# Performance work log

Hardware: AMD Instinct MI355X
Metric: run time of the kernel (lower is better)

Reference implementation:

```python
import jax, jax.numpy as jnp
import numpy as np

B, D, N, MH, MV = 4, 1024, 2048, 1024, 1024

def setup_inputs() -> dict:
    key = jax.random.key(0)
    k1, k2, k3, k4, k5 = jax.random.split(key, 5)
    return {
        "x": jax.random.normal(k1, (B, D, N), dtype=jnp.float32),
        "W_Q": jax.random.normal(k2, (MH, D), dtype=jnp.float32),
        "W_K": jax.random.normal(k3, (MH, D), dtype=jnp.float32),
        "W_V": jax.random.normal(k4, (MV, D), dtype=jnp.float32),
        "W_O": jax.random.normal(k5, (D, MV), dtype=jnp.float32),
    }

def reference(x, W_Q, W_K, W_V, W_O):
    # x: [b, d, n] (feature-major). Projections: [b, m, n]
    q = jnp.einsum('hd,bdn->bhn', W_Q, x)
    k = jnp.einsum('hd,bdn->bhn', W_K, x)
    v = jnp.einsum('vd,bdn->bvn', W_V, x)
    # scores[b,i,j] = sum_h k[b,h,i] * q[b,h,j]  -> [b, n, n]; NOTE: no 1/sqrt scale (faithful)
    scores = jnp.einsum('bhi,bhj->bij', k, q)
    scores = jax.nn.softmax(scores, axis=-1)
    # v @ scores -> [b, m_V, n]
    attn = jnp.einsum('bvi,bij->bvj', v, scores)
    # W_O @ attn -> [b, d, n]
    return jnp.einsum('dv,bvj->bdj', W_O, attn)
```

## Files before the change

### kernel.cpp

```cpp
#include <hip/hip_runtime.h>
#include <cstddef>
#include <cstdint>

typedef unsigned short u16;
typedef __attribute__((ext_vector_type(8))) short bf16x8;
typedef __attribute__((ext_vector_type(8))) _Float16 f16x8;
typedef __attribute__((ext_vector_type(4))) float f32x4;
typedef __attribute__((ext_vector_type(16))) float f32x16;

#define GLOBAL_AS __attribute__((address_space(1)))
#define LDS_AS __attribute__((address_space(3)))

__device__ __forceinline__ void async16(const u16* g, u16* l) {
    __builtin_amdgcn_global_load_lds((GLOBAL_AS const uint32_t*)g,
                                     (LDS_AS uint32_t*)l, 16, 0, 0);
}

__device__ __forceinline__ u16 f2bf(float f) {
    uint32_t u = __builtin_bit_cast(uint32_t, f);
    uint32_t r = (u + 0x7FFFu + ((u >> 16) & 1u)) >> 16;
    return (u16)r;
}

__global__ __launch_bounds__(256)
void wcast(const float4* __restrict__ src, u16* __restrict__ dst)
{
    int i = blockIdx.x * 256 + threadIdx.x;
    float4 v = src[i];
    ushort4 a = { f2bf(v.x), f2bf(v.y), f2bf(v.z), f2bf(v.w) };
    *(ushort4*)&dst[4 * (size_t)i] = a;
}

__global__ __launch_bounds__(256)
void tsplit_h2(const float* __restrict__ Sb, size_t sBatch,
               u16* __restrict__ Db, size_t dBatch, size_t plane,
               int R, int C)
{
    const float* S = Sb + blockIdx.z * sBatch;
    u16* D = Db + blockIdx.z * dBatch;
    __shared__ float t[32][33];
    int tx = threadIdx.x & 31, ty = threadIdx.x >> 5;
    int c0 = blockIdx.x * 32, r0 = blockIdx.y * 32;
    #pragma unroll
    for (int k = 0; k < 4; ++k)
        t[ty + 8 * k][tx] = S[(size_t)(r0 + ty + 8 * k) * C + c0 + tx];
    __syncthreads();
    #pragma unroll
    for (int k = 0; k < 4; ++k) {
        float a = t[tx][ty + 8 * k] * 64.0f;
        _Float16 h0 = (_Float16)a;
        _Float16 h1 = (_Float16)(a - (float)h0);
        size_t o = (size_t)(c0 + ty + 8 * k) * R + r0 + tx;
        D[o] = __builtin_bit_cast(u16, h0);
        D[plane + o] = __builtin_bit_cast(u16, h1);
    }
}

__global__ __launch_bounds__(256)
void xprep(const float* __restrict__ Sb, size_t sBatch,
           u16* __restrict__ BFb, size_t bfBatch,
           u16* __restrict__ Db, size_t dBatch, size_t plane)
{
    const float* S = Sb + blockIdx.z * sBatch;
    u16* BF = BFb + blockIdx.z * bfBatch;
    u16* D = Db + blockIdx.z * dBatch;
    __shared__ float t[32][33];
    int tx = threadIdx.x & 31, ty = threadIdx.x >> 5;
    int c0 = blockIdx.x * 32, r0 = blockIdx.y * 32;
    #pragma unroll
    for (int k = 0; k < 4; ++k) {
        float v = S[(size_t)(r0 + ty + 8 * k) * 2048 + c0 + tx];
        t[ty + 8 * k][tx] = v;
        BF[(size_t)(r0 + ty + 8 * k) * 2048 + c0 + tx] = f2bf(v);
    }
    __syncthreads();
    #pragma unroll
    for (int k = 0; k < 4; ++k) {
        float a = t[tx][ty + 8 * k] * 64.0f;
        _Float16 h0 = (_Float16)a;
        _Float16 h1 = (_Float16)(a - (float)h0);
        size_t o = (size_t)(c0 + ty + 8 * k) * 1024 + r0 + tx;
        D[o] = __builtin_bit_cast(u16, h0);
        D[plane + o] = __builtin_bit_cast(u16, h1);
    }
}

__global__ __launch_bounds__(256)
void tcast(const float* __restrict__ S, u16* __restrict__ D, int R, int C)
{
    __shared__ float t[32][33];
    int tx = threadIdx.x & 31, ty = threadIdx.x >> 5;
    int c0 = blockIdx.x * 32, r0 = blockIdx.y * 32;
    #pragma unroll
    for (int k = 0; k < 4; ++k)
        t[ty + 8 * k][tx] = S[(size_t)(r0 + ty + 8 * k) * C + c0 + tx];
    __syncthreads();
    #pragma unroll
    for (int k = 0; k < 4; ++k)
        D[(size_t)(c0 + ty + 8 * k) * R + r0 + tx] = f2bf(t[tx][ty + 8 * k]);
}

__global__ __launch_bounds__(256)
void tbf16(const u16* __restrict__ Sb, size_t sBatch, u16* __restrict__ Db, size_t dBatch)
{
    const u16* S = Sb + blockIdx.z * sBatch;
    u16* D = Db + blockIdx.z * dBatch;
    __shared__ u16 t[32][34];
    int tx = threadIdx.x & 31, ty = threadIdx.x >> 5;
    int c0 = blockIdx.x * 32, r0 = blockIdx.y * 32;
    #pragma unroll
    for (int k = 0; k < 4; ++k)
        t[ty + 8 * k][tx] = S[(size_t)(r0 + ty + 8 * k) * 2048 + c0 + tx];
    __syncthreads();
    #pragma unroll
    for (int k = 0; k < 4; ++k)
        D[(size_t)(c0 + ty + 8 * k) * 2048 + r0 + tx] = t[tx][ty + 8 * k];
}

#define MMF4(AF, BF)                                                                   \
    _Pragma("unroll") for (int i = 0; i < 4; ++i)                                      \
        _Pragma("unroll") for (int j = 0; j < 4; ++j)                                  \
            acc[i][j] = __builtin_amdgcn_mfma_f32_16x16x32_f16(AF[i], BF[j], acc[i][j], 0, 0, 0);
#define MMB4(AF, BF)                                                                   \
    _Pragma("unroll") for (int i = 0; i < 4; ++i)                                      \
        _Pragma("unroll") for (int j = 0; j < 4; ++j)                                  \
            acc[i][j] = __builtin_amdgcn_mfma_f32_16x16x32_bf16(AF[i], BF[j], acc[i][j], 0, 0, 0);

template<int TERMS, int EPI>
__global__ __launch_bounds__(256)
void gemm_big(const u16* __restrict__ Ab, size_t aBatch, size_t aPlane,
              const u16* __restrict__ Bb, size_t bBatch, size_t bPlane,
              void* __restrict__ Cb, size_t cBatch, size_t cPlane,
              int M, int N, int K)
{
    constexpr int RSZ = 4096;
    constexpr int BUF = (TERMS == 3 ? 4 : 2) * RSZ;
    __shared__ u16 lds[2 * BUF];
    const u16* A = Ab + blockIdx.z * aBatch;
    const u16* B = Bb + blockIdx.z * bBatch;
    const int tid = threadIdx.x;
    const int lane = tid & 63, wave = tid >> 6;
    const int m0 = blockIdx.y * 128, n0 = blockIdx.x * 128;
    const int l15 = lane & 15, q = lane >> 4;
    const int rm = (wave >> 1) * 64, rn = (wave & 1) * 64;

    int sr[2], sg[2], sbase[2];
    #pragma unroll
    for (int it = 0; it < 2; ++it) {
        int s = tid + it * 256;
        sr[it] = s >> 2;
        sg[it] = (s & 3) ^ ((sr[it] >> 1) & 3);
        sbase[it] = (it * 256 + wave * 64) * 8;
    }
    const int fsw = (q ^ ((l15 >> 1) & 3)) * 8;
    int aoff[4], boff[4];
    #pragma unroll
    for (int f = 0; f < 4; ++f) {
        aoff[f] = (rm + f * 16 + l15) * 32 + fsw;
        boff[f] = (rn + f * 16 + l15) * 32 + fsw;
    }

    f32x4 acc[4][4];
    #pragma unroll
    for (int i = 0; i < 4; ++i)
        #pragma unroll
        for (int j = 0; j < 4; ++j)
            acc[i][j] = (f32x4){0.f, 0.f, 0.f, 0.f};

#define STAGEB(PP, KT)                                                                 \
    do {                                                                               \
        _Pragma("unroll")                                                              \
        for (int it = 0; it < 2; ++it) {                                               \
            const size_t ao = (size_t)(m0 + sr[it]) * K + (KT) + sg[it] * 8;           \
            const size_t bo = (size_t)(n0 + sr[it]) * K + (KT) + sg[it] * 8;           \
            const int d = (PP) * BUF + sbase[it];                                      \
            if (TERMS == 3) {                                                          \
                async16(A + ao, &lds[d]);                                              \
                async16(A + aPlane + ao, &lds[d + RSZ]);                               \
                async16(B + bo, &lds[d + 2 * RSZ]);                                    \
                async16(B + bPlane + bo, &lds[d + 3 * RSZ]);                           \
            } else {                                                                   \
                async16(A + ao, &lds[d]);                                              \
                async16(B + bo, &lds[d + RSZ]);                                        \
            }                                                                          \
        }                                                                              \
    } while (0)

    STAGEB(0, 0);
    for (int kt = 0; kt < K; kt += 32) {
        const int p = (kt >> 5) & 1;
        __syncthreads();
        if (kt + 32 < K) STAGEB(p ^ 1, kt + 32);
        const u16* L = &lds[p * BUF];
        if (TERMS == 3) {
            f16x8 a0f[4], b0f[4], xf[4];
            #pragma unroll
            for (int f = 0; f < 4; ++f) a0f[f] = *(const f16x8*)&L[aoff[f]];
            #pragma unroll
            for (int f = 0; f < 4; ++f) b0f[f] = *(const f16x8*)&L[2 * RSZ + boff[f]];
            MMF4(a0f, b0f);
            #pragma unroll
            for (int f = 0; f < 4; ++f) xf[f] = *(const f16x8*)&L[3 * RSZ + boff[f]];
            MMF4(a0f, xf);
            #pragma unroll
            for (int f = 0; f < 4; ++f) xf[f] = *(const f16x8*)&L[RSZ + aoff[f]];
            MMF4(xf, b0f);
        } else {
            bf16x8 af[4], bf_[4];
            #pragma unroll
            for (int f = 0; f < 4; ++f) af[f] = *(const bf16x8*)&L[aoff[f]];
            #pragma unroll
            for (int f = 0; f < 4; ++f) bf_[f] = *(const bf16x8*)&L[RSZ + boff[f]];
            MMB4(af, bf_);
        }
    }
#undef STAGEB

    #pragma unroll
    for (int i = 0; i < 4; ++i) {
        int row = m0 + rm + i * 16 + q * 4;
        #pragma unroll
        for (int j = 0; j < 4; ++j) {
            int col = n0 + rn + j * 16 + l15;
            #pragma unroll
            for (int r = 0; r < 4; ++r) {
                float v = acc[i][j][r];
                size_t o = (size_t)(row + r) * N + col;
                if (EPI == 0) {
                    ((float*)Cb + blockIdx.z * cBatch)[o] = v;
                } else if (EPI == 1) {
                    u16* C0 = (u16*)Cb + blockIdx.z * cBatch;
                    float vs = v * 0.000244140625f;
                    _Float16 h0 = (_Float16)vs;
                    _Float16 h1 = (_Float16)(vs - (float)h0);
                    C0[o] = __builtin_bit_cast(u16, h0);
                    C0[cPlane + o] = __builtin_bit_cast(u16, h1);
                } else {
                    ((u16*)Cb + blockIdx.z * cBatch)[o] = f2bf(v);
                }
            }
        }
    }
}

template<int TERMS, int EPI, int TM, int TN, int WGM, int WGN>
__global__ __launch_bounds__(512, 2)
void gemm_w(const u16* __restrict__ Ab, size_t aBatch, size_t aPlane,
            const u16* __restrict__ Bb, size_t bBatch, size_t bPlane,
            void* __restrict__ Cb, size_t cBatch, size_t cPlane,
            int M, int N, int K)
{
    constexpr int ASZ = TM * 32;
    constexpr int BSZ = TN * 32;
    constexpr int APL = (TERMS == 3) ? 2 : 1;
    constexpr int BUF = APL * (ASZ + BSZ);
    constexpr int FM = TM / WGM / 32;
    constexpr int FN = TN / WGN / 32;
    constexpr int AIT = TM / 128;
    constexpr int BIT = TN / 128;
    extern __shared__ __align__(16) u16 lds[];

    int bid = blockIdx.x + gridDim.x * blockIdx.y;
    int cpr = gridDim.x >> 2;
    int c8 = bid & 7, kk = bid >> 3;
    int bx = (kk % cpr) * 4 + (c8 & 3);
    int by = (kk / cpr) * 2 + (c8 >> 2);

    const u16* A = Ab + blockIdx.z * aBatch;
    const u16* B = Bb + blockIdx.z * bBatch;
    const int tid = threadIdx.x;
    const int lane = tid & 63, wave = tid >> 6;
    const int m0 = by * TM, n0 = bx * TN;
    const int l31 = lane & 31, half = lane >> 5;
    const int rm = (wave / WGN) * (TM / WGM);
    const int rn = (wave % WGN) * (TN / WGN);

    int arow[FM], asw[FM], brow[FN], bsw[FN];
    #pragma unroll
    for (int f = 0; f < FM; ++f) { arow[f] = rm + f * 32 + l31; asw[f] = (arow[f] >> 1) & 3; }
    #pragma unroll
    for (int f = 0; f < FN; ++f) { brow[f] = rn + f * 32 + l31; bsw[f] = (brow[f] >> 1) & 3; }

    f32x16 acc[FM][FN];
    #pragma unroll
    for (int i = 0; i < FM; ++i)
        #pragma unroll
        for (int j = 0; j < FN; ++j)
            #pragma unroll
            for (int r = 0; r < 16; ++r) acc[i][j][r] = 0.f;

    auto stage = [&](int pp, int kt) {
        #pragma unroll
        for (int it = 0; it < AIT; ++it) {
            int s = tid + it * 512;
            int r = s >> 2;
            int g = (s & 3) ^ ((r >> 1) & 3);
            int base = pp * BUF + (it * 512 + wave * 64) * 8;
            size_t go = (size_t)(m0 + r) * K + kt + g * 8;
            async16(A + go, &lds[base]);
            if (TERMS == 3) async16(A + aPlane + go, &lds[base + ASZ]);
        }
        #pragma unroll
        for (int it = 0; it < BIT; ++it) {
            int s = tid + it * 512;
            int r = s >> 2;
            int g = (s & 3) ^ ((r >> 1) & 3);
            int base = pp * BUF + APL * ASZ + (it * 512 + wave * 64) * 8;
            size_t go = (size_t)(n0 + r) * K + kt + g * 8;
            async16(B + go, &lds[base]);
            if (TERMS == 3) async16(B + bPlane + go, &lds[base + BSZ]);
        }
    };

    stage(0, 0);
    for (int kt = 0; kt < K; kt += 32) {
        const int p = (kt >> 5) & 1;
        __syncthreads();
        if (kt + 32 < K) stage(p ^ 1, kt + 32);
        const u16* L = &lds[p * BUF];
        #pragma unroll
        for (int h = 0; h < 2; ++h) {
            if (TERMS == 3) {
                f16x8 a0[FM], b0[FN], tx[FM > FN ? FM : FN];
                #pragma unroll
                for (int f = 0; f < FM; ++f)
                    a0[f] = *(const f16x8*)&L[arow[f] * 32 + ((2 * h + half) ^ asw[f]) * 8];
                #pragma unroll
                for (int f = 0; f < FN; ++f)
                    b0[f] = *(const f16x8*)&L[APL * ASZ + brow[f] * 32 + ((2 * h + half) ^ bsw[f]) * 8];
                #pragma unroll
                for (int i = 0; i < FM; ++i)
                    #pragma unroll
                    for (int j = 0; j < FN; ++j)
                        acc[i][j] = __builtin_amdgcn_mfma_f32_32x32x16_f16(a0[i], b0[j], acc[i][j], 0, 0, 0);
                #pragma unroll
                for (int f = 0; f < FN; ++f)
                    tx[f] = *(const f16x8*)&L[APL * ASZ + BSZ + brow[f] * 32 + ((2 * h + half) ^ bsw[f]) * 8];
                #pragma unroll
                for (int i = 0; i < FM; ++i)
                    #pragma unroll
                    for (int j = 0; j < FN; ++j)
                        acc[i][j] = __builtin_amdgcn_mfma_f32_32x32x16_f16(a0[i], tx[j], acc[i][j], 0, 0, 0);
                #pragma unroll
                for (int f = 0; f < FM; ++f)
                    tx[f] = *(const f16x8*)&L[ASZ + arow[f] * 32 + ((2 * h + half) ^ asw[f]) * 8];
                #pragma unroll
                for (int i = 0; i < FM; ++i)
                    #pragma unroll
                    for (int j = 0; j < FN; ++j)
                        acc[i][j] = __builtin_amdgcn_mfma_f32_32x32x16_f16(tx[i], b0[j], acc[i][j], 0, 0, 0);
            } else {
                bf16x8 a0[FM], b0[FN];
                #pragma unroll
                for (int f = 0; f < FM; ++f)
                    a0[f] = *(const bf16x8*)&L[arow[f] * 32 + ((2 * h + half) ^ asw[f]) * 8];
                #pragma unroll
                for (int f = 0; f < FN; ++f)
                    b0[f] = *(const bf16x8*)&L[ASZ + brow[f] * 32 + ((2 * h + half) ^ bsw[f]) * 8];
                #pragma unroll
                for (int i = 0; i < FM; ++i)
                    #pragma unroll
                    for (int j = 0; j < FN; ++j)
                        acc[i][j] = __builtin_amdgcn_mfma_f32_32x32x16_bf16(a0[i], b0[j], acc[i][j], 0, 0, 0);
            }
        }
    }

    #pragma unroll
    for (int i = 0; i < FM; ++i) {
        #pragma unroll
        for (int j = 0; j < FN; ++j) {
            int col = n0 + rn + j * 32 + l31;
            #pragma unroll
            for (int r = 0; r < 16; ++r) {
                int row = m0 + rm + i * 32 + (r & 3) + 8 * (r >> 2) + 4 * half;
                float v = acc[i][j][r];
                size_t o = (size_t)row * N + col;
                if (EPI == 0) {
                    ((float*)Cb + blockIdx.z * cBatch)[o] = v;
                } else if (EPI == 1) {
                    u16* C0 = (u16*)Cb + blockIdx.z * cBatch;
                    float vs = v * 0.000244140625f;
                    _Float16 h0 = (_Float16)vs;
                    _Float16 h1 = (_Float16)(vs - (float)h0);
                    C0[o] = __builtin_bit_cast(u16, h0);
                    C0[cPlane + o] = __builtin_bit_cast(u16, h1);
                } else {
                    ((u16*)Cb + blockIdx.z * cBatch)[o] = f2bf(v);
                }
            }
        }
    }
}

__global__ __launch_bounds__(256)
void softmax_p(const float* __restrict__ Sb, size_t sBatch, u16* __restrict__ Pb, size_t pBatch)
{
    const float* S = Sb + blockIdx.y * sBatch + (size_t)blockIdx.x * 2048;
    u16* P = Pb + blockIdx.y * pBatch + (size_t)blockIdx.x * 2048;
    const int tid = threadIdx.x;

    float4 v0 = *(const float4*)&S[tid * 4];
    float4 v1 = *(const float4*)&S[1024 + tid * 4];

    float m = fmaxf(fmaxf(fmaxf(v0.x, v0.y), fmaxf(v0.z, v0.w)),
                    fmaxf(fmaxf(v1.x, v1.y), fmaxf(v1.z, v1.w)));
    #pragma unroll
    for (int off = 32; off > 0; off >>= 1)
        m = fmaxf(m, __shfl_xor(m, off, 64));
    __shared__ float redm[4];
    if ((tid & 63) == 0) redm[tid >> 6] = m;
    __syncthreads();
    m = fmaxf(fmaxf(redm[0], redm[1]), fmaxf(redm[2], redm[3]));

    v0.x = __expf(v0.x - m); v0.y = __expf(v0.y - m);
    v0.z = __expf(v0.z - m); v0.w = __expf(v0.w - m);
    v1.x = __expf(v1.x - m); v1.y = __expf(v1.y - m);
    v1.z = __expf(v1.z - m); v1.w = __expf(v1.w - m);

    float s = v0.x + v0.y + v0.z + v0.w + v1.x + v1.y + v1.z + v1.w;
    #pragma unroll
    for (int off = 32; off > 0; off >>= 1)
        s += __shfl_xor(s, off, 64);
    __shared__ float reds[4];
    if ((tid & 63) == 0) reds[tid >> 6] = s;
    __syncthreads();
    s = reds[0] + reds[1] + reds[2] + reds[3];

    const float r = 1.0f / s;
    ushort4 o0 = { f2bf(v0.x * r), f2bf(v0.y * r), f2bf(v0.z * r), f2bf(v0.w * r) };
    ushort4 o1 = { f2bf(v1.x * r), f2bf(v1.y * r), f2bf(v1.z * r), f2bf(v1.w * r) };
    *(ushort4*)&P[tid * 4] = o0;
    *(ushort4*)&P[1024 + tid * 4] = o1;
}

extern "C" void kernel_launch(void* const* d_in, const int* in_sizes, int n_in,
                              void* d_out, int out_size, void* d_ws, size_t ws_size,
                              hipStream_t stream)
{
    const size_t MB = 1048576;
    const size_t WREG = 34 * MB;
    const size_t PER  = 32 * MB;
    const size_t PER_US = PER / 2, PER_F = PER / 4;

    char* ws = (char*)d_ws;
    u16* WQT2 = (u16*)ws;
    u16* WKT2 = (u16*)(ws + 4 * MB);
    u16* M2   = (u16*)(ws + 8 * MB);
    u16* WObf = (u16*)(ws + 12 * MB);
    u16* WVT  = (u16*)(ws + 14 * MB);
    u16* WOV  = (u16*)(ws + 16 * MB);
    u16* xbf  = (u16*)(ws + 18 * MB);

    int G = (ws_size >= WREG + 4 * PER) ? 4 : (ws_size >= WREG + 2 * PER) ? 2 : 1;

    const float* x = (const float*)d_in[0];
    float* out = (float*)d_out;
    dim3 blk(256);

    hipFuncSetAttribute((const void*)gemm_w<3, 0, 256, 256, 2, 4>,
                        hipFuncAttributeMaxDynamicSharedMemorySize, 131072);
    hipFuncSetAttribute((const void*)gemm_w<3, 1, 256, 128, 4, 2>,
                        hipFuncAttributeMaxDynamicSharedMemorySize, 98304);

    tsplit_h2<<<dim3(32, 32, 1), blk, 0, stream>>>((const float*)d_in[1], 0, WQT2, 0, 1048576, 1024, 1024);
    tsplit_h2<<<dim3(32, 32, 1), blk, 0, stream>>>((const float*)d_in[2], 0, WKT2, 0, 1048576, 1024, 1024);
    gemm_big<3, 1><<<dim3(8, 8, 1), blk, 0, stream>>>(WKT2, 0, 1048576, WQT2, 0, 1048576,
                                                      M2, 0, 1048576, 1024, 1024, 1024);
    wcast<<<1024, blk, 0, stream>>>((const float4*)d_in[4], WObf);
    tcast<<<dim3(32, 32, 1), blk, 0, stream>>>((const float*)d_in[3], WVT, 1024, 1024);
    gemm_big<1, 2><<<dim3(8, 8, 1), blk, 0, stream>>>(WObf, 0, 0, WVT, 0, 0,
                                                      WOV, 0, 0, 1024, 1024, 1024);

    for (int b0 = 0; b0 < 4; b0 += G) {
        char* R = ws + WREG;
        u16*   xT2 = (u16*)R;
        u16*   TT2 = (u16*)(R + 8 * MB);
        float* S32 = (float*)(R + 16 * MB);
        u16*   Pb  = (u16*)R;
        u16*   PTb = (u16*)(R + 8 * MB);
        u16*   XPT = (u16*)(R + 16 * MB);

        xprep<<<dim3(64, 32, G), blk, 0, stream>>>(x + (size_t)b0 * 2097152, 2097152,
                                                   xbf + (size_t)b0 * 2097152, 2097152,
                                                   xT2, PER_US, 2097152);
        gemm_w<3, 1, 256, 128, 4, 2><<<dim3(8, 8, G), 512, 98304, stream>>>(
            xT2, PER_US, 2097152, M2, 0, 1048576, TT2, PER_US, 2097152, 2048, 1024, 1024);
        gemm_w<3, 0, 256, 256, 2, 4><<<dim3(8, 8, G), 512, 131072, stream>>>(
            xT2, PER_US, 2097152, TT2, PER_US, 2097152, S32, PER_F, 0, 2048, 2048, 1024);
        softmax_p<<<dim3(2048, G), blk, 0, stream>>>(S32, PER_F, Pb, PER_US);
        tbf16<<<dim3(64, 64, G), blk, 0, stream>>>(Pb, PER_US, PTb, PER_US);
        gemm_w<1, 2, 256, 128, 4, 2><<<dim3(8, 8, G), 512, 49152, stream>>>(
            PTb, PER_US, 0, xbf + (size_t)b0 * 2097152, 2097152, 0,
            XPT, PER_US, 0, 2048, 1024, 2048);
        gemm_w<1, 0, 256, 128, 4, 2><<<dim3(16, 4, G), 512, 49152, stream>>>(
            WOV, 0, 0, XPT, PER_US, 0, out + (size_t)b0 * 2097152, 2097152, 0,
            1024, 2048, 1024);
    }
}
```

Baseline: 420.6 us.

## Add pipelined 3-term split-fp16 GEMM with staggered per-plane prefetch and grouped tiles

Adds a new gemm_p6 kernel for the two 3-term split-fp16 GEMMs (T projection and scores). It replaces the single-barrier double buffer with per-plane staged async loads, issued between MFMA phases, using explicit vmcnt waits, s_barriers and setprio. It also adds a block-id swizzle so neighbouring blocks share tiles in cache, and caps occupancy with launch_bounds(512,2). The aim is to overlap global-to-LDS traffic with MFMA work and cut stalls from the full __syncthreads per K-step, at the cost of hand-tuned waitcnt counts that must match the load pattern exactly.

Result: no change. 419.1 us (-0.3%).

```diff
diff --git a/kernel.cpp b/kernel.cpp
--- a/kernel.cpp
+++ b/kernel.cpp
@@ -21,6 +21,8 @@
     uint32_t r = (u + 0x7FFFu + ((u >> 16) & 1u)) >> 16;
     return (u16)r;
 }
+
+#define VMC(N) asm volatile("s_waitcnt vmcnt(" #N ")" ::: "memory")
 
 __global__ __launch_bounds__(256)
 void wcast(const float4* __restrict__ src, u16* __restrict__ dst)
@@ -320,49 +322,18 @@
         const u16* L = &lds[p * BUF];
         #pragma unroll
         for (int h = 0; h < 2; ++h) {
-            if (TERMS == 3) {
-                f16x8 a0[FM], b0[FN], tx[FM > FN ? FM : FN];
+            bf16x8 a0[FM], b0[FN];
+            #pragma unroll
+            for (int f = 0; f < FM; ++f)
+                a0[f] = *(const bf16x8*)&L[arow[f] * 32 + ((2 * h + half) ^ asw[f]) * 8];
+            #pragma unroll
+            for (int f = 0; f < FN; ++f)
+                b0[f] = *(const bf16x8*)&L[ASZ + brow[f] * 32 + ((2 * h + half) ^ bsw[f]) * 8];
+            #pragma unroll
+            for (int i = 0; i < FM; ++i)
                 #pragma unroll
-                for (int f = 0; f < FM; ++f)
-                    a0[f] = *(const f16x8*)&L[arow[f] * 32 + ((2 * h + half) ^ asw[f]) * 8];
-                #pragma unroll
-                for (int f = 0; f < FN; ++f)
-                    b0[f] = *(const f16x8*)&L[APL * ASZ + brow[f] * 32 + ((2 * h + half) ^ bsw[f]) * 8];
-                #pragma unroll
-                for (int i = 0; i < FM; ++i)
-                    #pragma unroll
-                    for (int j = 0; j < FN; ++j)
-                        acc[i][j] = __builtin_amdgcn_mfma_f32_32x32x16_f16(a0[i], b0[j], acc[i][j], 0, 0, 0);
-                #pragma unroll
-                for (int f = 0; f < FN; ++f)
-                    tx[f] = *(const f16x8*)&L[APL * ASZ + BSZ + brow[f] * 32 + ((2 * h + half) ^ bsw[f]) * 8];
-                #pragma unroll
-                for (int i = 0; i < FM; ++i)
-                    #pragma unroll
-                    for (int j = 0; j < FN; ++j)
-                        acc[i][j] = __builtin_amdgcn_mfma_f32_32x32x16_f16(a0[i], tx[j], acc[i][j], 0, 0, 0);
-                #pragma unroll
-                for (int f = 0; f < FM; ++f)
-                    tx[f] = *(const f16x8*)&L[ASZ + arow[f] * 32 + ((2 * h + half) ^ asw[f]) * 8];
-                #pragma unroll
-                for (int i = 0; i < FM; ++i)
-                    #pragma unroll
-                    for (int j = 0; j < FN; ++j)
-                        acc[i][j] = __builtin_amdgcn_mfma_f32_32x32x16_f16(tx[i], b0[j], acc[i][j], 0, 0, 0);
-            } else {
-                bf16x8 a0[FM], b0[FN];
-                #pragma unroll
-                for (int f = 0; f < FM; ++f)
-                    a0[f] = *(const bf16x8*)&L[arow[f] * 32 + ((2 * h + half) ^ asw[f]) * 8];
-                #pragma unroll
-                for (int f = 0; f < FN; ++f)
-                    b0[f] = *(const bf16x8*)&L[ASZ + brow[f] * 32 + ((2 * h + half) ^ bsw[f]) * 8];
-                #pragma unroll
-                for (int i = 0; i < FM; ++i)
-                    #pragma unroll
-                    for (int j = 0; j < FN; ++j)
-                        acc[i][j] = __builtin_amdgcn_mfma_f32_32x32x16_bf16(a0[i], b0[j], acc[i][j], 0, 0, 0);
-            }
+                for (int j = 0; j < FN; ++j)
+                    acc[i][j] = __builtin_amdgcn_mfma_f32_32x32x16_bf16(a0[i], b0[j], acc[i][j], 0, 0, 0);
         }
     }
 
@@ -393,6 +364,197 @@
     }
 }
 
+template<int EPI, int TM, int TN, int WGM, int WGN>
+__global__ __launch_bounds__(512, 2)
+void gemm_p6(const u16* __restrict__ Ab, size_t aBatch, size_t aPlane,
+             const u16* __restrict__ Bb, size_t bBatch, size_t bPlane,
+             void* __restrict__ Cb, size_t cBatch, size_t cPlane,
+             int M, int N, int K)
+{
+    constexpr int ASZ = TM * 32;
+    constexpr int BSZ = TN * 32;
+    constexpr int BUFU = 2 * (ASZ + BSZ);
+    constexpr int FM = TM / WGM / 32;
+    constexpr int FN = TN / WGN / 32;
+    constexpr int LA = TM / 128;
+    constexpr int LB = TN / 128;
+    constexpr int NBND = LA + 2 * LB;
+    static_assert(NBND == 6 || NBND == 4, "unexpected vmcnt constant");
+    extern __shared__ __align__(16) u16 lds[];
+
+    int bid = blockIdx.x + gridDim.x * blockIdx.y;
+    int cpr = gridDim.x >> 2;
+    int c8 = bid & 7, kk = bid >> 3;
+    int bx = (kk % cpr) * 4 + (c8 & 3);
+    int by = (kk / cpr) * 2 + (c8 >> 2);
+
+    const u16* A = Ab + blockIdx.z * aBatch;
+    const u16* B = Bb + blockIdx.z * bBatch;
+    const int tid = threadIdx.x;
+    const int lane = tid & 63, wave = tid >> 6;
+    const int m0 = by * TM, n0 = bx * TN;
+    const int l31 = lane & 31, half = lane >> 5;
+    const int rm = (wave / WGN) * (TM / WGM);
+    const int rn = (wave % WGN) * (TN / WGN);
+
+    int arow[FM], asw[FM], brow[FN], bsw[FN];
+    #pragma unroll
+    for (int f = 0; f < FM; ++f) { arow[f] = rm + f * 32 + l31; asw[f] = (arow[f] >> 1) & 3; }
+    #pragma unroll
+    for (int f = 0; f < FN; ++f) { brow[f] = rn + f * 32 + l31; bsw[f] = (brow[f] >> 1) & 3; }
+
+    f32x16 acc[FM][FN];
+    #pragma unroll
+    for (int i = 0; i < FM; ++i)
+        #pragma unroll
+        for (int j = 0; j < FN; ++j)
+            #pragma unroll
+            for (int r = 0; r < 16; ++r) acc[i][j][r] = 0.f;
+
+    auto stA = [&](int t, const u16* sp, int uoff) {
+        const int pp = (t & 1) * BUFU;
+        const int kt = t << 5;
+        #pragma unroll
+        for (int it = 0; it < LA; ++it) {
+            int s = tid + it * 512;
+            int r = s >> 2;
+            int g = (s & 3) ^ ((r >> 1) & 3);
+            size_t go = (size_t)(m0 + r) * K + kt + g * 8;
+            async16(sp + go, &lds[pp + uoff + (it * 512 + wave * 64) * 8]);
+        }
+    };
+    auto stB = [&](int t, const u16* sp, int uoff) {
+        const int pp = (t & 1) * BUFU;
+        const int kt = t << 5;
+        #pragma unroll
+        for (int it = 0; it < LB; ++it) {
+            int s = tid + it * 512;
+            int r = s >> 2;
+            int g = (s & 3) ^ ((r >> 1) & 3);
+            size_t go = (size_t)(n0 + r) * K + kt + g * 8;
+            async16(sp + go, &lds[pp + uoff + (it * 512 + wave * 64) * 8]);
+        }
+    };
+
+    const int NT = K >> 5;
+
+    stA(0, A, 0);
+    stB(0, B, 2 * ASZ);
+    stB(0, B + bPlane, 2 * ASZ + BSZ);
+    stA(0, A + aPlane, ASZ);
+    if (NT > 1) {
+        stA(1, A, 0);
+        stB(1, B, 2 * ASZ);
+        stB(1, B + bPlane, 2 * ASZ + BSZ);
+        if constexpr (NBND == 6) VMC(6); else VMC(4);
+    } else {
+        VMC(0);
+    }
+    __builtin_amdgcn_sched_barrier(0);
+    __builtin_amdgcn_s_barrier();
+
+    for (int t = 0; t < NT; ++t) {
+        const u16* L = &lds[(t & 1) * BUFU];
+        f16x8 a0r[FM][2], b0r[FN][2];
+
+        #pragma unroll
+        for (int h = 0; h < 2; ++h) {
+            #pragma unroll
+            for (int f = 0; f < FM; ++f)
+                a0r[f][h] = *(const f16x8*)&L[arow[f] * 32 + ((2 * h + half) ^ asw[f]) * 8];
+            #pragma unroll
+            for (int f = 0; f < FN; ++f)
+                b0r[f][h] = *(const f16x8*)&L[2 * ASZ + brow[f] * 32 + ((2 * h + half) ^ bsw[f]) * 8];
+        }
+        if (t + 1 < NT) stA(t + 1, A + aPlane, ASZ);
+        __builtin_amdgcn_s_barrier();
+        __builtin_amdgcn_s_setprio(1);
+        #pragma unroll
+        for (int h = 0; h < 2; ++h)
+            #pragma unroll
+            for (int i = 0; i < FM; ++i)
+                #pragma unroll
+                for (int j = 0; j < FN; ++j)
+                    acc[i][j] = __builtin_amdgcn_mfma_f32_32x32x16_f16(a0r[i][h], b0r[j][h], acc[i][j], 0, 0, 0);
+        __builtin_amdgcn_s_setprio(0);
+        __builtin_amdgcn_s_barrier();
+
+        {
+            f16x8 tr[FN][2];
+            #pragma unroll
+            for (int h = 0; h < 2; ++h)
+                #pragma unroll
+                for (int f = 0; f < FN; ++f)
+                    tr[f][h] = *(const f16x8*)&L[2 * ASZ + BSZ + brow[f] * 32 + ((2 * h + half) ^ bsw[f]) * 8];
+            if (t + 2 < NT) { stA(t + 2, A, 0); stB(t + 2, B, 2 * ASZ); }
+            __builtin_amdgcn_s_barrier();
+            __builtin_amdgcn_s_setprio(1);
+            #pragma unroll
+            for (int h = 0; h < 2; ++h)
+                #pragma unroll
+                for (int i = 0; i < FM; ++i)
+                    #pragma unroll
+                    for (int j = 0; j < FN; ++j)
+                        acc[i][j] = __builtin_amdgcn_mfma_f32_32x32x16_f16(a0r[i][h], tr[j][h], acc[i][j], 0, 0, 0);
+            __builtin_amdgcn_s_setprio(0);
+            __builtin_amdgcn_s_barrier();
+        }
+
+        {
+            f16x8 tr[FM][2];
+            #pragma unroll
+            for (int h = 0; h < 2; ++h)
+                #pragma unroll
+                for (int f = 0; f < FM; ++f)
+                    tr[f][h] = *(const f16x8*)&L[ASZ + arow[f] * 32 + ((2 * h + half) ^ asw[f]) * 8];
+            if (t + 2 < NT) stB(t + 2, B + bPlane, 2 * ASZ + BSZ);
+            __builtin_amdgcn_s_barrier();
+            __builtin_amdgcn_s_setprio(1);
+            #pragma unroll
+            for (int h = 0; h < 2; ++h)
+                #pragma unroll
+                for (int i = 0; i < FM; ++i)
+                    #pragma unroll
+                    for (int j = 0; j < FN; ++j)
+                        acc[i][j] = __builtin_amdgcn_mfma_f32_32x32x16_f16(tr[i][h], b0r[j][h], acc[i][j], 0, 0, 0);
+            __builtin_amdgcn_s_setprio(0);
+            if (t + 2 < NT) {
+                if constexpr (NBND == 6) VMC(6); else VMC(4);
+            } else if (t + 1 < NT) {
+                VMC(0);
+            }
+            __builtin_amdgcn_sched_barrier(0);
+            __builtin_amdgcn_s_barrier();
+        }
+    }
+
+    #pragma unroll
+    for (int i = 0; i < FM; ++i) {
+        #pragma unroll
+        for (int j = 0; j < FN; ++j) {
+            int col = n0 + rn + j * 32 + l31;
+            #pragma unroll
+            for (int r = 0; r < 16; ++r) {
+                int row = m0 + rm + i * 32 + (r & 3) + 8 * (r >> 2) + 4 * half;
+                float v = acc[i][j][r];
+                size_t o = (size_t)row * N + col;
+                if (EPI == 0) {
+                    ((float*)Cb + blockIdx.z * cBatch)[o] = v;
+                } else if (EPI == 1) {
+                    u16* C0 = (u16*)Cb + blockIdx.z * cBatch;
+                    float vs = v * 0.000244140625f;
+                    _Float16 h0 = (_Float16)vs;
+                    _Float16 h1 = (_Float16)(vs - (float)h0);
+                    C0[o] = __builtin_bit_cast(u16, h0);
+                    C0[cPlane + o] = __builtin_bit_cast(u16, h1);
+                } else {
+                    ((u16*)Cb + blockIdx.z * cBatch)[o] = f2bf(v);
+                }
+            }
+        }
+    }
+}
+
 __global__ __launch_bounds__(256)
 void softmax_p(const float* __restrict__ Sb, size_t sBatch, u16* __restrict__ Pb, size_t pBatch)
 {
@@ -458,9 +620,9 @@
     float* out = (float*)d_out;
     dim3 blk(256);
 
-    hipFuncSetAttribute((const void*)gemm_w<3, 0, 256, 256, 2, 4>,
+    hipFuncSetAttribute((const void*)gemm_p6<0, 256, 256, 2, 4>,
                         hipFuncAttributeMaxDynamicSharedMemorySize, 131072);
-    hipFuncSetAttribute((const void*)gemm_w<3, 1, 256, 128, 4, 2>,
+    hipFuncSetAttribute((const void*)gemm_p6<1, 256, 128, 4, 2>,
                         hipFuncAttributeMaxDynamicSharedMemorySize, 98304);
 
     tsplit_h2<<<dim3(32, 32, 1), blk, 0, stream>>>((const float*)d_in[1], 0, WQT2, 0, 1048576, 1024, 1024);
@@ -484,9 +646,9 @@
         xprep<<<dim3(64, 32, G), blk, 0, stream>>>(x + (size_t)b0 * 2097152, 2097152,
                                                    xbf + (size_t)b0 * 2097152, 2097152,
                                                    xT2, PER_US, 2097152);
-        gemm_w<3, 1, 256, 128, 4, 2><<<dim3(8, 8, G), 512, 98304, stream>>>(
+        gemm_p6<1, 256, 128, 4, 2><<<dim3(8, 8, G), 512, 98304, stream>>>(
             xT2, PER_US, 2097152, M2, 0, 1048576, TT2, PER_US, 2097152, 2048, 1024, 1024);
-        gemm_w<3, 0, 256, 256, 2, 4><<<dim3(8, 8, G), 512, 131072, stream>>>(
+        gemm_p6<0, 256, 256, 2, 4><<<dim3(8, 8, G), 512, 131072, stream>>>(
             xT2, PER_US, 2097152, TT2, PER_US, 2097152, S32, PER_F, 0, 2048, 2048, 1024);
         softmax_p<<<dim3(2048, G), blk, 0, stream>>>(S32, PER_F, Pb, PER_US);
         tbf16<<<dim3(64, 64, G), blk, 0, stream>>>(Pb, PER_US, PTb, PER_US);
```
